# Kernel tuning notes

Measured on AMD Instinct MI355X. Metric: run time of the kernel, lower is better.

The kernel has to match this reference:

```python
import jax, jax.numpy as jnp
import numpy as np

HIDDEN = 1024
HEADS = 16
HEAD_DIM = HIDDEN // HEADS  # 64
RP_DIM = 256
KERNEL_EPS = 1e-3


def _gaussian_orthogonal_matrix(nb_rows, nb_cols, seed=0):
    """Orthogonal random features (scaling=0), as in Performer FAVOR+."""
    rng = np.random.RandomState(seed)
    blocks = []
    n_full = nb_rows // nb_cols
    for _ in range(n_full):
        q, _ = np.linalg.qr(rng.randn(nb_cols, nb_cols))
        blocks.append(q.T)
    rem = nb_rows - n_full * nb_cols
    if rem > 0:
        q, _ = np.linalg.qr(rng.randn(nb_cols, nb_cols))
        blocks.append(q.T[:rem])
    mat = np.concatenate(blocks, axis=0)
    # scaling=0: row norms drawn from chi distribution (norms of gaussian rows)
    multiplier = np.linalg.norm(rng.randn(nb_rows, nb_cols), axis=1)
    return (multiplier[:, None] * mat).astype(np.float32)


def setup_inputs() -> dict:
    key = jax.random.key(0)
    kx, kw = jax.random.split(key)
    x = jax.random.normal(kx, (4, 4096, HIDDEN), dtype=jnp.float32)
    w_qkv = jax.random.normal(kw, (HIDDEN, 3 * HIDDEN), dtype=jnp.float32) * 0.02
    b_qkv = jnp.zeros((3 * HIDDEN,), dtype=jnp.float32)
    proj = jnp.asarray(_gaussian_orthogonal_matrix(RP_DIM, HEAD_DIM))  # [M, Dh]
    return {"x": x, "w_qkv": w_qkv, "b_qkv": b_qkv, "proj": proj}


def reference(x, w_qkv, b_qkv, proj):
    B, N, _ = x.shape
    qkv = x @ w_qkv + b_qkv  # [B, N, 3*hidden]
    q, k, v = jnp.split(qkv, 3, axis=-1)

    def to_heads(t):
        return t.reshape(B, N, HEADS, HEAD_DIM).transpose(0, 2, 1, 3)  # bhnd

    q, k, v = to_heads(q), to_heads(k), to_heads(v)

    # forward scales by d**-0.25, generalized_kernel normalizes by d**-0.25 again
    scale = HEAD_DIM ** -0.5
    # generalized kernel features: relu(x_norm @ proj^T) + eps  -> [B,H,N,M]
    q_prime = jax.nn.relu(jnp.einsum('bhnd,md->bhnm', q * scale, proj)) + KERNEL_EPS
    k_prime = jax.nn.relu(jnp.einsum('bhnd,md->bhnm', k * scale, proj)) + KERNEL_EPS

    # non-causal linear attention
    k_sum = k_prime.sum(axis=2)  # [B,H,M]
    d_inv = 1.0 / jnp.einsum('bhnm,bhm->bhn', q_prime, k_sum)  # [B,H,N]
    context = jnp.einsum('bhnm,bhnd->bhmd', k_prime, v)  # [B,H,M,Dh]
    out = jnp.einsum('bhmd,bhnm,bhn->bhnd', context, q_prime, d_inv)

    out = out.transpose(0, 2, 1, 3).reshape(B, N, HIDDEN)
    return out
```

## Files before the change

kernel.cpp:

```cpp
#include <hip/hip_runtime.h>

#define B_   4
#define N_   4096
#define NH   16
#define DH   64
#define HID  1024
#define NC3  3072
#define M_   256
#define BH   64
#define SCALE 0.125f
#define EPS   1e-3f
#define CH2  8
#define CH3  16

typedef _Float16 half8  __attribute__((ext_vector_type(8)));
typedef _Float16 half4v __attribute__((ext_vector_type(4)));
typedef float floatx4   __attribute__((ext_vector_type(4)));

#define GLD_LDS16(gptr, lds_base) \
  __builtin_amdgcn_global_load_lds((const __attribute__((address_space(1))) void*)(gptr), \
                                   (__attribute__((address_space(3))) void*)(lds_base), 16, 0, 0)

__global__ __launch_bounds__(256) void convert_xh(
    const float* __restrict__ x, _Float16* __restrict__ xh)
{
    const size_t i = ((size_t)blockIdx.x * 256 + threadIdx.x) * 8;
    float4 a = *(const float4*)(x + i);
    float4 b = *(const float4*)(x + i + 4);
    half8 h;
    h[0] = (_Float16)a.x; h[1] = (_Float16)a.y; h[2] = (_Float16)a.z; h[3] = (_Float16)a.w;
    h[4] = (_Float16)b.x; h[5] = (_Float16)b.y; h[6] = (_Float16)b.z; h[7] = (_Float16)b.w;
    *(half8*)(xh + i) = h;
}

__global__ __launch_bounds__(256) void convert_wT(
    const float* __restrict__ w, _Float16* __restrict__ wT)
{
    __shared__ float t[64][65];
    const int tid = threadIdx.x;
    const int kb = blockIdx.y * 64, nb = blockIdx.x * 64;
    const int c = tid & 63, r0 = tid >> 6;
#pragma unroll
    for (int rr = 0; rr < 64; rr += 4)
        t[rr + r0][c] = w[(size_t)(kb + rr + r0) * NC3 + nb + c];
    __syncthreads();
    const float sc = (nb < 2048) ? SCALE : 1.0f;
#pragma unroll
    for (int rr = 0; rr < 64; rr += 4)
        wT[(size_t)(nb + rr + r0) * HID + kb + c] = (_Float16)(t[c][rr + r0] * sc);
}

__global__ __launch_bounds__(256) void convert_projh(
    const float* __restrict__ proj, _Float16* __restrict__ projh)
{
    const int i = blockIdx.x * 256 + threadIdx.x;
    projh[i] = (_Float16)proj[i];
}

__device__ __forceinline__ void stage_tile_qkv(
    const _Float16* __restrict__ xh, const _Float16* __restrict__ wT,
    int row0, int col0, int kt, char* ab, char* bb, int wv, int srow, int sblk)
{
    const size_t ko = (size_t)kt * 64;
#pragma unroll
    for (int s = 0; s < 4; ++s) {
        const int r = s * 64 + srow;
        GLD_LDS16(xh + (size_t)(row0 + r) * HID + ko + 8 * sblk, ab + s * 8192 + wv * 1024);
        GLD_LDS16(wT + (size_t)(col0 + r) * HID + ko + 8 * sblk, bb + s * 8192 + wv * 1024);
    }
}

__global__ __launch_bounds__(512, 2) void gemm_qkv_mfma(
    const _Float16* __restrict__ xh, const _Float16* __restrict__ wT,
    const float* __restrict__ bias,
    _Float16* __restrict__ qh, _Float16* __restrict__ kh, _Float16* __restrict__ vTh)
{
    __shared__ __align__(16) char smem[131072];

    const int tid  = threadIdx.x;
    const int lane = tid & 63;
    const int wv   = tid >> 6;
    const int wm   = wv >> 2;
    const int wn   = wv & 3;
    const int lr   = lane & 15;
    const int lg   = lane >> 4;
    const int lr7  = lr & 7;

    const int bid  = blockIdx.x;
    const int tile = ((bid & 7) * 96) + (bid >> 3);
    const int tm   = tile / 12;
    const int tn   = tile - tm * 12;
    const int row0 = tm * 256;
    const int col0 = tn * 256;

    const int srow = 8 * wv + (lane >> 3);
    const int sblk = (lane & 7) ^ (lane >> 3);

    char* buf0A = smem;
    char* buf0B = smem + 32768;
    char* buf1A = smem + 65536;
    char* buf1B = smem + 98304;

    floatx4 acc[8][4] = {};

    stage_tile_qkv(xh, wT, row0, col0, 0, buf0A, buf0B, wv, srow, sblk);
    stage_tile_qkv(xh, wT, row0, col0, 1, buf1A, buf1B, wv, srow, sblk);

    for (int t = 0; t < 16; ++t) {
        if (t < 15) asm volatile("s_waitcnt vmcnt(8)" ::: "memory");
        else        asm volatile("s_waitcnt vmcnt(0)" ::: "memory");
        __builtin_amdgcn_s_barrier();
        __builtin_amdgcn_sched_barrier(0);

        char* ab = (t & 1) ? buf1A : buf0A;
        char* bb = (t & 1) ? buf1B : buf0B;

        half8 af[4], bf[4];

#pragma unroll
        for (int i = 0; i < 4; ++i)
            af[i] = *(const half8*)(ab + (wm * 128 + 16 * i + lr) * 128 + ((lg ^ lr7) * 16));
#pragma unroll
        for (int j = 0; j < 4; ++j)
            bf[j] = *(const half8*)(bb + (wn * 64 + 16 * j + lr) * 128 + ((lg ^ lr7) * 16));
        __builtin_amdgcn_s_setprio(1);
#pragma unroll
        for (int i = 0; i < 4; ++i)
#pragma unroll
            for (int j = 0; j < 4; ++j)
                acc[i][j] = __builtin_amdgcn_mfma_f32_16x16x32_f16(af[i], bf[j], acc[i][j], 0, 0, 0);
        __builtin_amdgcn_s_setprio(0);
        __builtin_amdgcn_s_barrier();
        __builtin_amdgcn_sched_barrier(0);

#pragma unroll
        for (int i = 0; i < 4; ++i)
            af[i] = *(const half8*)(ab + (wm * 128 + 16 * (4 + i) + lr) * 128 + ((lg ^ lr7) * 16));
        __builtin_amdgcn_s_setprio(1);
#pragma unroll
        for (int i = 0; i < 4; ++i)
#pragma unroll
            for (int j = 0; j < 4; ++j)
                acc[4 + i][j] = __builtin_amdgcn_mfma_f32_16x16x32_f16(af[i], bf[j], acc[4 + i][j], 0, 0, 0);
        __builtin_amdgcn_s_setprio(0);
        __builtin_amdgcn_s_barrier();
        __builtin_amdgcn_sched_barrier(0);

#pragma unroll
        for (int i = 0; i < 4; ++i)
            af[i] = *(const half8*)(ab + (wm * 128 + 16 * i + lr) * 128 + (((4 + lg) ^ lr7) * 16));
#pragma unroll
        for (int j = 0; j < 4; ++j)
            bf[j] = *(const half8*)(bb + (wn * 64 + 16 * j + lr) * 128 + (((4 + lg) ^ lr7) * 16));
        __builtin_amdgcn_s_setprio(1);
#pragma unroll
        for (int i = 0; i < 4; ++i)
#pragma unroll
            for (int j = 0; j < 4; ++j)
                acc[i][j] = __builtin_amdgcn_mfma_f32_16x16x32_f16(af[i], bf[j], acc[i][j], 0, 0, 0);
        __builtin_amdgcn_s_setprio(0);
        __builtin_amdgcn_s_barrier();
        __builtin_amdgcn_sched_barrier(0);

#pragma unroll
        for (int i = 0; i < 4; ++i)
            af[i] = *(const half8*)(ab + (wm * 128 + 16 * (4 + i) + lr) * 128 + (((4 + lg) ^ lr7) * 16));
        asm volatile("s_waitcnt lgkmcnt(0)" ::: "memory");
        __builtin_amdgcn_sched_barrier(0);
        __builtin_amdgcn_s_barrier();
        __builtin_amdgcn_sched_barrier(0);
        if (t < 14)
            stage_tile_qkv(xh, wT, row0, col0, t + 2, ab, bb, wv, srow, sblk);
        __builtin_amdgcn_sched_barrier(0);
        __builtin_amdgcn_s_setprio(1);
#pragma unroll
        for (int i = 0; i < 4; ++i)
#pragma unroll
            for (int j = 0; j < 4; ++j)
                acc[4 + i][j] = __builtin_amdgcn_mfma_f32_16x16x32_f16(af[i], bf[j], acc[4 + i][j], 0, 0, 0);
        __builtin_amdgcn_s_setprio(0);
    }

#pragma unroll
    for (int j = 0; j < 4; ++j) {
        const int col = col0 + wn * 64 + 16 * j + lr;
        const int which = col >> 10;
        const int h = (col >> 6) & 15;
        const int d = col & 63;
        const float bb2 = bias[col] * ((which < 2) ? SCALE : 1.0f);
        if (which == 2) {
#pragma unroll
            for (int i = 0; i < 8; ++i) {
                const int m0 = row0 + wm * 128 + 16 * i + 4 * lg;
                const int bi = m0 >> 12, n0 = m0 & (N_ - 1);
                half4v hv;
#pragma unroll
                for (int rg = 0; rg < 4; ++rg) hv[rg] = (_Float16)(acc[i][j][rg] + bb2);
                *(half4v*)(vTh + ((size_t)(bi * NH + h) * DH + d) * N_ + n0) = hv;
            }
        } else {
            _Float16* dst = (which == 0) ? qh : kh;
#pragma unroll
            for (int i = 0; i < 8; ++i)
#pragma unroll
                for (int rg = 0; rg < 4; ++rg) {
                    const int m = row0 + wm * 128 + 16 * i + 4 * lg + rg;
                    const int bi = m >> 12, n = m & (N_ - 1);
                    dst[((size_t)(bi * NH + h) * N_ + n) * DH + d] =
                        (_Float16)(acc[i][j][rg] + bb2);
                }
        }
    }
}

__global__ __launch_bounds__(256) void kv_ctx_mfma(
    const _Float16* __restrict__ kh, const _Float16* __restrict__ vTh,
    const _Float16* __restrict__ projh,
    float* __restrict__ ctx_part, float* __restrict__ ksum_part)
{
    __shared__ __align__(16) _Float16 Kt[64 * 64];
    __shared__ __align__(16) _Float16 Vt[64 * 64];
    __shared__ __align__(16) _Float16 Sp[256 * 64];

    const int tid  = threadIdx.x;
    const int lane = tid & 63;
    const int wv   = tid >> 6;
    const int lr = lane & 15, lg = lane >> 4;
    const int bh = blockIdx.y, chunk = blockIdx.x;
    const int n_base = chunk * (N_ / CH2);

    half8 bfP[4][2];
#pragma unroll
    for (int j = 0; j < 4; ++j)
#pragma unroll
        for (int ks = 0; ks < 2; ++ks)
            bfP[j][ks] = *(const half8*)(projh + (size_t)(64 * wv + 16 * j + lr) * DH + 32 * ks + 8 * lg);

    floatx4 cacc[4][4] = {};
    float ks_acc[4] = {0.f, 0.f, 0.f, 0.f};

    for (int t = 0; t < (N_ / CH2) / 64; ++t) {
        const int n0 = n_base + t * 64;
        __syncthreads();
#pragma unroll
        for (int s = 0; s < 2; ++s) {
            const int R = wv * 16 + s * 8;
            const int r = R + (lane >> 3);
            const int db = (lane & 7) ^ (r & 7);
            GLD_LDS16(kh + ((size_t)(bh * N_ + n0 + r)) * DH + db * 8, (char*)Kt + R * 128);
        }
#pragma unroll
        for (int s = 0; s < 2; ++s) {
            const int R = wv * 16 + s * 8;
            const int r = R + (lane >> 3);
            const int db = (lane & 7) ^ (r & 7);
            GLD_LDS16(vTh + ((size_t)(bh * DH + r)) * N_ + n0 + db * 8, (char*)Vt + R * 128);
        }
        __syncthreads();

        floatx4 s[4][4] = {};
#pragma unroll
        for (int ks = 0; ks < 2; ++ks) {
            half8 aK[4];
#pragma unroll
            for (int i = 0; i < 4; ++i) {
                const int r = 16 * i + lr;
                aK[i] = *(const half8*)((const char*)Kt + r * 128 + (((4 * ks + lg) ^ (r & 7)) * 16));
            }
#pragma unroll
            for (int i = 0; i < 4; ++i)
#pragma unroll
                for (int j = 0; j < 4; ++j)
                    s[i][j] = __builtin_amdgcn_mfma_f32_16x16x32_f16(aK[i], bfP[j][ks], s[i][j], 0, 0, 0);
        }
#pragma unroll
        for (int i = 0; i < 4; ++i)
#pragma unroll
            for (int j = 0; j < 4; ++j) {
                const int m = 64 * wv + 16 * j + lr;
                const int nn0 = 16 * i + 4 * lg;
                half4v h4;
#pragma unroll
                for (int rg = 0; rg < 4; ++rg) {
                    const float kv = fmaxf(s[i][j][rg], 0.f) + EPS;
                    ks_acc[j] += kv;
                    h4[rg] = (_Float16)kv;
                }
                const int db = nn0 >> 3, sub = nn0 & 7;
                *(half4v*)((char*)Sp + m * 128 + ((db ^ (m & 7)) * 16) + sub * 2) = h4;
            }
#pragma unroll
        for (int ks = 0; ks < 2; ++ks) {
            half8 aV[4], bS[4];
#pragma unroll
            for (int i = 0; i < 4; ++i) {
                const int r = 16 * i + lr;
                aV[i] = *(const half8*)((const char*)Vt + r * 128 + (((4 * ks + lg) ^ (r & 7)) * 16));
            }
#pragma unroll
            for (int j = 0; j < 4; ++j) {
                const int m = 64 * wv + 16 * j + lr;
                bS[j] = *(const half8*)((const char*)Sp + m * 128 + (((4 * ks + lg) ^ (m & 7)) * 16));
            }
#pragma unroll
            for (int i = 0; i < 4; ++i)
#pragma unroll
                for (int j = 0; j < 4; ++j)
                    cacc[i][j] = __builtin_amdgcn_mfma_f32_16x16x32_f16(aV[i], bS[j], cacc[i][j], 0, 0, 0);
        }
    }

#pragma unroll
    for (int i = 0; i < 4; ++i)
#pragma unroll
        for (int j = 0; j < 4; ++j)
#pragma unroll
            for (int rg = 0; rg < 4; ++rg) {
                const int d = 16 * i + 4 * lg + rg;
                const int m = 64 * wv + 16 * j + lr;
                ctx_part[(((size_t)chunk * BH + bh) * DH + d) * M_ + m] = cacc[i][j][rg];
            }
#pragma unroll
    for (int j = 0; j < 4; ++j) {
        float v = ks_acc[j];
        v += __shfl_xor(v, 16);
        v += __shfl_xor(v, 32);
        if (lg == 0)
            ksum_part[((size_t)chunk * BH + bh) * M_ + 64 * wv + 16 * j + lr] = v;
    }
}

__global__ __launch_bounds__(256) void reduce_ctx(
    const float* __restrict__ ctx_part, const float* __restrict__ ksum_part,
    _Float16* __restrict__ ctxTh, _Float16* __restrict__ ksumh)
{
    const int idx = blockIdx.x * 256 + threadIdx.x;
    const int CTX = BH * DH * M_;
    if (idx < CTX) {
        float sum = 0.f;
#pragma unroll
        for (int c = 0; c < CH2; ++c) sum += ctx_part[(size_t)c * CTX + idx];
        ctxTh[idx] = (_Float16)sum;
    } else {
        const int kidx = idx - CTX;
        if (kidx < BH * M_) {
            float sum = 0.f;
#pragma unroll
            for (int c = 0; c < CH2; ++c) sum += ksum_part[(size_t)c * BH * M_ + kidx];
            ksumh[kidx] = (_Float16)sum;
        }
    }
}

__global__ __launch_bounds__(256) void attn_out_mfma(
    const _Float16* __restrict__ qh, const _Float16* __restrict__ projh,
    const _Float16* __restrict__ ctxTh, const _Float16* __restrict__ ksumh,
    float* __restrict__ out)
{
    __shared__ __align__(16) _Float16 Sp[64 * 256];

    const int tid  = threadIdx.x;
    const int lane = tid & 63;
    const int wv   = tid >> 6;
    const int lr = lane & 15, lg = lane >> 4;
    const int bh = blockIdx.y;
    const int bi = bh >> 4, h = bh & 15;
    const int n_base = blockIdx.x * (N_ / CH3);

    half8 afP[4][2];
#pragma unroll
    for (int I = 0; I < 4; ++I)
#pragma unroll
        for (int ks = 0; ks < 2; ++ks)
            afP[I][ks] = *(const half8*)(projh + (size_t)(64 * wv + 16 * I + lr) * DH + 32 * ks + 8 * lg);

    for (int t = 0; t < (N_ / CH3) / 64; ++t) {
        const int n0 = n_base + t * 64;
        __syncthreads();
        floatx4 sacc[4][4] = {};
#pragma unroll
        for (int ks = 0; ks < 2; ++ks) {
            half8 bq[4];
#pragma unroll
            for (int J = 0; J < 4; ++J)
                bq[J] = *(const half8*)(qh + ((size_t)bh * N_ + n0 + 16 * J + lr) * DH + 32 * ks + 8 * lg);
#pragma unroll
            for (int I = 0; I < 4; ++I)
#pragma unroll
                for (int J = 0; J < 4; ++J)
                    sacc[I][J] = __builtin_amdgcn_mfma_f32_16x16x32_f16(afP[I][ks], bq[J], sacc[I][J], 0, 0, 0);
        }
#pragma unroll
        for (int I = 0; I < 4; ++I)
#pragma unroll
            for (int J = 0; J < 4; ++J) {
                const int n = 16 * J + lr;
                const int m0 = 64 * wv + 16 * I + 4 * lg;
                half4v h4;
#pragma unroll
                for (int rg = 0; rg < 4; ++rg)
                    h4[rg] = (_Float16)(fmaxf(sacc[I][J][rg], 0.f) + EPS);
                const int db = m0 >> 3, sub = m0 & 7;
                *(half4v*)((char*)Sp + n * 512 + ((db ^ (n & 31)) * 16) + sub * 2) = h4;
            }
        __syncthreads();
        floatx4 oacc[4] = {};
        floatx4 dacc = {};
        const int nl = 16 * wv + lr;
#pragma unroll
        for (int ks = 0; ks < 8; ++ks) {
            half8 aq = *(const half8*)((const char*)Sp + nl * 512 + (((4 * ks + lg) ^ (nl & 31)) * 16));
#pragma unroll
            for (int j = 0; j < 4; ++j) {
                half8 bc = *(const half8*)(ctxTh + ((size_t)bh * DH + 16 * j + lr) * M_ + 32 * ks + 8 * lg);
                oacc[j] = __builtin_amdgcn_mfma_f32_16x16x32_f16(aq, bc, oacc[j], 0, 0, 0);
            }
            half8 bk = {};
            if (lr == 0)
                bk = *(const half8*)(ksumh + (size_t)bh * M_ + 32 * ks + 8 * lg);
            dacc = __builtin_amdgcn_mfma_f32_16x16x32_f16(aq, bk, dacc, 0, 0, 0);
        }
#pragma unroll
        for (int rg = 0; rg < 4; ++rg) {
            float den = dacc[rg];
            den = __shfl(den, lane & 48);
            const float dinv = 1.f / den;
            const int n = n0 + 16 * wv + 4 * lg + rg;
#pragma unroll
            for (int j = 0; j < 4; ++j)
                out[(((size_t)bi * N_ + n) * NH + h) * DH + 16 * j + lr] = oacc[j][rg] * dinv;
        }
    }
}

extern "C" void kernel_launch(void* const* d_in, const int* in_sizes, int n_in,
                              void* d_out, int out_size, void* d_ws, size_t ws_size,
                              hipStream_t stream) {
    const float* x    = (const float*)d_in[0];
    const float* w    = (const float*)d_in[1];
    const float* bias = (const float*)d_in[2];
    const float* proj = (const float*)d_in[3];
    float* out = (float*)d_out;
    char* ws = (char*)d_ws;

    const size_t XN  = (size_t)B_ * N_ * HID;
    const size_t QKV = (size_t)BH * N_ * DH;
    const size_t CTX = (size_t)BH * DH * M_;

    _Float16* xh       = (_Float16*)ws;                          ws += XN * 2;
    _Float16* wT       = (_Float16*)ws;                          ws += NC3 * HID * 2;
    _Float16* projh    = (_Float16*)ws;                          ws += M_ * DH * 2;
    _Float16* qh       = (_Float16*)ws;                          ws += QKV * 2;
    _Float16* kh       = (_Float16*)ws;                          ws += QKV * 2;
    _Float16* vTh      = (_Float16*)ws;                          ws += QKV * 2;
    _Float16* ctxTh    = (_Float16*)ws;                          ws += CTX * 2;
    _Float16* ksumh    = (_Float16*)ws;                          ws += BH * M_ * 2;
    float*    ctx_part = (float*)ws;                             ws += (size_t)CH2 * CTX * 4;
    float*    ksum_part= (float*)ws;                             ws += (size_t)CH2 * BH * M_ * 4;

    convert_xh<<<dim3(XN / (256 * 8)), 256, 0, stream>>>(x, xh);
    convert_wT<<<dim3(NC3 / 64, HID / 64), 256, 0, stream>>>(w, wT);
    convert_projh<<<dim3(M_ * DH / 256), 256, 0, stream>>>(proj, projh);

    gemm_qkv_mfma<<<dim3(768), dim3(512), 0, stream>>>(xh, wT, bias, qh, kh, vTh);

    kv_ctx_mfma<<<dim3(CH2, BH), 256, 0, stream>>>(kh, vTh, projh, ctx_part, ksum_part);

    reduce_ctx<<<dim3((CTX + BH * M_ + 255) / 256), 256, 0, stream>>>(ctx_part, ksum_part, ctxTh, ksumh);

    attn_out_mfma<<<dim3(CH3, BH), 256, 0, stream>>>(qh, projh, ctxTh, ksumh, out);
}
```

Measured before the change: 367.7 us.

## Restructure QKV GEMM inner loop into two k-halves with fewer barriers

Replaces the four quarter-step phases of the QKV projection GEMM main loop, each separated by a workgroup barrier and sched_barrier, with two k-half phases. Each phase loads all 8 A fragments and 4 B fragments from LDS up front, then issues 32 MFMAs. Barriers become inline-asm s_barrier and the sched_barrier fences are removed, giving the compiler freedom to interleave LDS reads with MFMAs. The cost is higher register pressure from holding 24 half8 fragments live at once, plus less explicit control over scheduling.

```diff
diff --git a/kernel.cpp b/kernel.cpp
--- a/kernel.cpp
+++ b/kernel.cpp
@@ -21,6 +21,8 @@
   __builtin_amdgcn_global_load_lds((const __attribute__((address_space(1))) void*)(gptr), \
                                    (__attribute__((address_space(3))) void*)(lds_base), 16, 0, 0)
 
+#define SBAR() asm volatile("s_barrier" ::: "memory")
+
 __global__ __launch_bounds__(256) void convert_xh(
     const float* __restrict__ x, _Float16* __restrict__ xh)
 {
@@ -109,75 +111,46 @@
     for (int t = 0; t < 16; ++t) {
         if (t < 15) asm volatile("s_waitcnt vmcnt(8)" ::: "memory");
         else        asm volatile("s_waitcnt vmcnt(0)" ::: "memory");
-        __builtin_amdgcn_s_barrier();
-        __builtin_amdgcn_sched_barrier(0);
+        SBAR();
 
         char* ab = (t & 1) ? buf1A : buf0A;
         char* bb = (t & 1) ? buf1B : buf0B;
 
-        half8 af[4], bf[4];
-
-#pragma unroll
-        for (int i = 0; i < 4; ++i)
-            af[i] = *(const half8*)(ab + (wm * 128 + 16 * i + lr) * 128 + ((lg ^ lr7) * 16));
+        half8 a0[8], b0[4];
+#pragma unroll
+        for (int i = 0; i < 8; ++i)
+            a0[i] = *(const half8*)(ab + (wm * 128 + 16 * i + lr) * 128 + ((lg ^ lr7) * 16));
 #pragma unroll
         for (int j = 0; j < 4; ++j)
-            bf[j] = *(const half8*)(bb + (wn * 64 + 16 * j + lr) * 128 + ((lg ^ lr7) * 16));
+            b0[j] = *(const half8*)(bb + (wn * 64 + 16 * j + lr) * 128 + ((lg ^ lr7) * 16));
+
         __builtin_amdgcn_s_setprio(1);
 #pragma unroll
-        for (int i = 0; i < 4; ++i)
+        for (int i = 0; i < 8; ++i)
 #pragma unroll
             for (int j = 0; j < 4; ++j)
-                acc[i][j] = __builtin_amdgcn_mfma_f32_16x16x32_f16(af[i], bf[j], acc[i][j], 0, 0, 0);
+                acc[i][j] = __builtin_amdgcn_mfma_f32_16x16x32_f16(a0[i], b0[j], acc[i][j], 0, 0, 0);
         __builtin_amdgcn_s_setprio(0);
-        __builtin_amdgcn_s_barrier();
-        __builtin_amdgcn_sched_barrier(0);
-
-#pragma unroll
-        for (int i = 0; i < 4; ++i)
-            af[i] = *(const half8*)(ab + (wm * 128 + 16 * (4 + i) + lr) * 128 + ((lg ^ lr7) * 16));
-        __builtin_amdgcn_s_setprio(1);
-#pragma unroll
-        for (int i = 0; i < 4; ++i)
-#pragma unroll
-            for (int j = 0; j < 4; ++j)
-                acc[4 + i][j] = __builtin_amdgcn_mfma_f32_16x16x32_f16(af[i], bf[j], acc[4 + i][j], 0, 0, 0);
-        __builtin_amdgcn_s_setprio(0);
-        __builtin_amdgcn_s_barrier();
-        __builtin_amdgcn_sched_barrier(0);
-
-#pragma unroll
-        for (int i = 0; i < 4; ++i)
-            af[i] = *(const half8*)(ab + (wm * 128 + 16 * i + lr) * 128 + (((4 + lg) ^ lr7) * 16));
+
+        half8 a1[8], b1[4];
+#pragma unroll
+        for (int i = 0; i < 8; ++i)
+            a1[i] = *(const half8*)(ab + (wm * 128 + 16 * i + lr) * 128 + (((4 + lg) ^ lr7) * 16));
 #pragma unroll
         for (int j = 0; j < 4; ++j)
-            bf[j] = *(const half8*)(bb + (wn * 64 + 16 * j + lr) * 128 + (((4 + lg) ^ lr7) * 16));
-        __builtin_amdgcn_s_setprio(1);
-#pragma unroll
-        for (int i = 0; i < 4; ++i)
-#pragma unroll
-            for (int j = 0; j < 4; ++j)
-                acc[i][j] = __builtin_amdgcn_mfma_f32_16x16x32_f16(af[i], bf[j], acc[i][j], 0, 0, 0);
-        __builtin_amdgcn_s_setprio(0);
-        __builtin_amdgcn_s_barrier();
-        __builtin_amdgcn_sched_barrier(0);
-
-#pragma unroll
-        for (int i = 0; i < 4; ++i)
-            af[i] = *(const half8*)(ab + (wm * 128 + 16 * (4 + i) + lr) * 128 + (((4 + lg) ^ lr7) * 16));
+            b1[j] = *(const half8*)(bb + (wn * 64 + 16 * j + lr) * 128 + (((4 + lg) ^ lr7) * 16));
+
         asm volatile("s_waitcnt lgkmcnt(0)" ::: "memory");
-        __builtin_amdgcn_sched_barrier(0);
-        __builtin_amdgcn_s_barrier();
-        __builtin_amdgcn_sched_barrier(0);
+        SBAR();
         if (t < 14)
             stage_tile_qkv(xh, wT, row0, col0, t + 2, ab, bb, wv, srow, sblk);
-        __builtin_amdgcn_sched_barrier(0);
+
         __builtin_amdgcn_s_setprio(1);
 #pragma unroll
-        for (int i = 0; i < 4; ++i)
+        for (int i = 0; i < 8; ++i)
 #pragma unroll
             for (int j = 0; j < 4; ++j)
-                acc[4 + i][j] = __builtin_amdgcn_mfma_f32_16x16x32_f16(af[i], bf[j], acc[4 + i][j], 0, 0, 0);
+                acc[i][j] = __builtin_amdgcn_mfma_f32_16x16x32_f16(a1[i], b1[j], acc[i][j], 0, 0, 0);
         __builtin_amdgcn_s_setprio(0);
     }
 
```

Result: faster. 359.5 us (-2.2%).
